# Kernel tuning notes

Hardware: AMD Instinct MI355X
Metric: run time of the kernel (lower is better)

Reference implementation:

```python
import jax, jax.numpy as jnp
import numpy as np

M_DIM, Z_DIM, C = 256, 128, 32
N, L = 512, 384


def setup_inputs() -> dict:
    key = jax.random.key(0)
    ks = jax.random.split(key, 9)
    s = 1.0 / np.sqrt(M_DIM)
    return {
        "m": jax.random.normal(ks[0], (N, L, M_DIM), dtype=jnp.float32),
        "ln_gamma": jnp.ones((M_DIM,), jnp.float32),
        "ln_beta": jnp.zeros((M_DIM,), jnp.float32),
        "w1": jax.random.normal(ks[1], (M_DIM, C), jnp.float32) * s,
        "b1": jnp.zeros((C,), jnp.float32),
        "w2": jax.random.normal(ks[2], (M_DIM, C), jnp.float32) * s,
        "b2": jnp.zeros((C,), jnp.float32),
        "w3": jax.random.normal(ks[3], (C * C, Z_DIM), jnp.float32) * (1.0 / np.sqrt(C * C)),
        "b3": jnp.zeros((Z_DIM,), jnp.float32),
    }


def _layernorm(x, gamma, beta, eps=1e-5):
    mu = jnp.mean(x, axis=-1, keepdims=True)
    var = jnp.mean(jnp.square(x - mu), axis=-1, keepdims=True)
    return (x - mu) * jax.lax.rsqrt(var + eps) * gamma + beta


def reference(m, ln_gamma, ln_beta, w1, b1, w2, b2, w3, b3):
    n = m.shape[0]
    o = _layernorm(m, ln_gamma, ln_beta)          # (N, L, D)
    a = o @ w2 + b2                                # (N, L, C)  linear2
    b = o @ w1 + b1                                # (N, L, C)  linear1
    # mean over N of outer products: reassociated as a single contraction over n
    op = jnp.einsum('nia,njb->ijab', a, b) / n     # (L, L, C, C)
    ll = op.shape[0]
    z = op.reshape(ll, ll, -1) @ w3 + b3           # (L, L, Z)
    return z
```

## Files before the change

kernel.cpp:

```cpp
#include <hip/hip_runtime.h>
#include <hip/hip_bf16.h>
#include <stdint.h>

#define L_DIM 384
#define MD    256
#define CC    32
#define ZD    128
#define NB    512
#define K2    1024
#define MROWS 12288

typedef __attribute__((ext_vector_type(4))) float  f32x4;
typedef __attribute__((ext_vector_type(8))) short  bf16x8;

typedef __attribute__((address_space(1))) unsigned char* gcp;
typedef __attribute__((address_space(3))) unsigned char* lcp;

#define SBAR()  __builtin_amdgcn_s_barrier()
#define LGKM0() asm volatile("s_waitcnt lgkmcnt(0)" ::: "memory")
#define VMW(n)  asm volatile("s_waitcnt vmcnt(" #n ")" ::: "memory")
#define PRIO1() __builtin_amdgcn_s_setprio(1)
#define PRIO0() __builtin_amdgcn_s_setprio(0)

__device__ __forceinline__ unsigned short f2bf(float x) {
    union { float f; unsigned u; } v; v.f = x;
    unsigned r = v.u + 0x7fffu + ((v.u >> 16) & 1u);
    return (unsigned short)(r >> 16);
}

__device__ __forceinline__ uint2 pack4(unsigned short a, unsigned short b,
                                       unsigned short c, unsigned short d) {
    uint2 r; r.x = (unsigned)a | ((unsigned)b << 16);
    r.y = (unsigned)c | ((unsigned)d << 16); return r;
}

__global__ __launch_bounds__(256) void prep_kernel(
    const float* __restrict__ w1, const float* __restrict__ w2,
    const float* __restrict__ w3,
    unsigned short* __restrict__ w3frag, unsigned short* __restrict__ wfrag)
{
    int idx = blockIdx.x * 256 + threadIdx.x;
    if (idx < 131072) {
        int e = idx & 7, lane = (idx >> 3) & 63, zg = (idx >> 9) & 7, ks = idx >> 12;
        int k2p = ks * 32 + ((lane >> 4) << 3) + e;
        int wrow = (k2p & 31) * 32 + (k2p >> 5);
        int z  = zg * 16 + (lane & 15);
        w3frag[idx] = f2bf(w3[(size_t)wrow * ZD + z]);
    } else {
        int j = idx - 131072;
        int e = j & 7, lane = (j >> 3) & 63, nf = (j >> 9) & 3, ks = j >> 11;
        int c = nf * 16 + (lane & 15);
        int d = ks * 32 + ((lane >> 4) << 3) + e;
        float v = (c < CC) ? w2[d * CC + c] : w1[d * CC + (c - CC)];
        wfrag[j] = f2bf(v);
    }
}

__global__ __launch_bounds__(256, 4) void ln_proj_kernel(
    const float* __restrict__ mm, const float* __restrict__ gamma, const float* __restrict__ beta,
    const unsigned short* __restrict__ wfrag,
    const float* __restrict__ b1, const float* __restrict__ b2,
    unsigned short* __restrict__ At, unsigned short* __restrict__ Bt)
{
    __shared__ alignas(16) char o_b[32768];

    const int tid = threadIdx.x, wv = tid >> 6, lane = tid & 63;
    const int l0 = blockIdx.y * 2;
    const int n0 = blockIdx.x * 32;

    const int l_loc = wv >> 1;
    const int nbase = (wv & 1) << 4;
    const int l_g = l0 + l_loc;
    f32x4 g4 = *(const f32x4*)(gamma + lane * 4);
    f32x4 e4 = *(const f32x4*)(beta + lane * 4);

    #pragma unroll 4
    for (int r = 0; r < 16; ++r) {
        int row_loc = wv * 16 + r;
        int n_g = n0 + nbase + r;
        const float* src = mm + ((size_t)n_g * L_DIM + l_g) * MD + lane * 4;
        f32x4 x = *(const f32x4*)src;
        float s  = x[0] + x[1] + x[2] + x[3];
        float s2 = x[0]*x[0] + x[1]*x[1] + x[2]*x[2] + x[3]*x[3];
        #pragma unroll
        for (int off = 32; off > 0; off >>= 1) {
            s  += __shfl_xor(s,  off);
            s2 += __shfl_xor(s2, off);
        }
        float mu  = s * (1.0f / MD);
        float var = s2 * (1.0f / MD) - mu * mu;
        float rs  = rsqrtf(var + 1e-5f);
        unsigned short o0 = f2bf((x[0] - mu) * rs * g4[0] + e4[0]);
        unsigned short o1 = f2bf((x[1] - mu) * rs * g4[1] + e4[1]);
        unsigned short o2 = f2bf((x[2] - mu) * rs * g4[2] + e4[2]);
        unsigned short o3 = f2bf((x[3] - mu) * rs * g4[3] + e4[3]);
        *(uint2*)(o_b + row_loc * 512 + ((lane * 8) ^ ((row_loc & 7) << 4))) = pack4(o0, o1, o2, o3);
    }

    f32x4 acc[4] = {{0,0,0,0},{0,0,0,0},{0,0,0,0},{0,0,0,0}};
    const int lrow = lane & 15;
    const int kq16 = (lane >> 4) << 4;
    const int arow = wv * 16 + lrow;
    #pragma unroll
    for (int ks = 0; ks < 8; ++ks) {
        bf16x8 a = *(const bf16x8*)(o_b + arow * 512 + ((ks * 64 + kq16) ^ ((arow & 7) << 4)));
        #pragma unroll
        for (int nf = 0; nf < 4; ++nf) {
            bf16x8 b = *(const bf16x8*)(wfrag + (size_t)((ks * 4 + nf) * 64 + lane) * 8);
            acc[nf] = __builtin_amdgcn_mfma_f32_16x16x32_bf16(a, b, acc[nf], 0, 0, 0);
        }
    }

    const int rr0 = wv * 16 + ((lane >> 4) << 2);
    const int n_gw = n0 + (rr0 & 31);
    const int l_gw = l0 + (rr0 >> 5);
    #pragma unroll
    for (int nf = 0; nf < 4; ++nf) {
        int c = nf * 16 + lrow;
        float bias = (c < CC) ? b2[c] : b1[c - CC];
        unsigned short ob0 = f2bf(acc[nf][0] + bias);
        unsigned short ob1 = f2bf(acc[nf][1] + bias);
        unsigned short ob2 = f2bf(acc[nf][2] + bias);
        unsigned short ob3 = f2bf(acc[nf][3] + bias);
        unsigned short* dst = ((c < CC) ? At : Bt) + (size_t)(l_gw * CC + (c & 31)) * NB + n_gw;
        *(uint2*)dst = pack4(ob0, ob1, ob2, ob3);
    }
}

__global__ __launch_bounds__(512, 2) void opm_kernel(
    const unsigned short* __restrict__ At, const unsigned short* __restrict__ Bt,
    const unsigned short* __restrict__ w3frag, const float* __restrict__ b3,
    float* __restrict__ Z)
{
    __shared__ alignas(128) char smem[131072];
    char* const Ab = smem;
    char* const Bb = smem + 65536;

    const int tid = threadIdx.x, wv = tid >> 6, lane = tid & 63;

    const int lin = blockIdx.y * 48 + blockIdx.x;
    const int xcd = lin & 7, chunk = lin >> 3;
    const int i0 = (xcd * 6 + (chunk % 6)) * 256;
    const int j0 = (chunk / 6) * 256;

    const int lrow = lane & 15;
    const int kq16 = (lane >> 4) << 4;
    const int wr = (wv >> 2) * 128, wc = (wv & 3) * 64;

    auto stage = [&](const unsigned short* __restrict__ src, int tile0, int kt,
                     int half, int isA) {
        #pragma unroll
        for (int q = 0; q < 2; ++q) {
            int rl0 = q * 64 + wv * 8;
            int rl  = rl0 + (lane >> 3);
            int rc  = isA ? ((rl  & 63) + ((rl  >> 6) << 7) + half * 64)
                          : ((rl  & 31) + ((rl  >> 5) << 6) + half * 32);
            int rc0 = isA ? ((rl0 & 63) + ((rl0 >> 6) << 7) + half * 64)
                          : ((rl0 & 31) + ((rl0 >> 5) << 6) + half * 32);
            const unsigned short* g = src + (size_t)(tile0 + rc) * NB + kt * 64
                                      + (((lane & 7) ^ (lane >> 3)) << 3);
            char* l = (isA ? Ab : Bb) + (kt & 1) * 32768 + rc0 * 128;
            __builtin_amdgcn_global_load_lds((gcp)g, (lcp)l, 16, 0, 0);
        }
    };

    f32x4 acc[8][4] = {};
    bf16x8 av[8], bl[4], bh[4];

    auto rdA = [&](const char* ab, int qrow) {
        #pragma unroll
        for (int mfl = 0; mfl < 4; ++mfl) {
            int row = wr + qrow * 64 + mfl * 16 + lrow;
            const char* p = ab + row * 128;
            av[mfl*2+0] = *(const bf16x8*)(p + ((     kq16) ^ ((row & 7) << 4)));
            av[mfl*2+1] = *(const bf16x8*)(p + ((64 + kq16) ^ ((row & 7) << 4)));
        }
    };
    auto rdB = [&](const char* bb, int qcol, bf16x8* bv) {
        #pragma unroll
        for (int nfl = 0; nfl < 2; ++nfl) {
            int col = wc + qcol * 32 + nfl * 16 + lrow;
            const char* p = bb + col * 128;
            bv[nfl*2+0] = *(const bf16x8*)(p + ((     kq16) ^ ((col & 7) << 4)));
            bv[nfl*2+1] = *(const bf16x8*)(p + ((64 + kq16) ^ ((col & 7) << 4)));
        }
    };
    auto MM = [&](bf16x8* bv, int mbase, int nbase) {
        #pragma unroll
        for (int mfl = 0; mfl < 4; ++mfl)
            #pragma unroll
            for (int nfl = 0; nfl < 2; ++nfl)
                #pragma unroll
                for (int ks = 0; ks < 2; ++ks)
                    acc[mbase+mfl][nbase+nfl] = __builtin_amdgcn_mfma_f32_16x16x32_bf16(
                        av[mfl*2+ks], bv[nfl*2+ks], acc[mbase+mfl][nbase+nfl], 0, 0, 0);
    };

    stage(At, i0, 0, 0, 1); stage(At, i0, 0, 1, 1);
    stage(Bt, j0, 0, 0, 0); stage(Bt, j0, 0, 1, 0);
    stage(At, i0, 1, 0, 1); stage(At, i0, 1, 1, 1);
    stage(Bt, j0, 1, 0, 0); stage(Bt, j0, 1, 1, 0);
    VMW(8);
    SBAR();

    const char* a0 = Ab;           const char* b0 = Bb;
    const char* a1 = Ab + 32768;   const char* b1 = Bb + 32768;

    for (int t = 0; t < 3; ++t) {
        const int ktc = 2*t + 2, ktd = 2*t + 3;
        rdA(a0, 0); rdB(b0, 0, bl);
        SBAR(); LGKM0(); PRIO1(); MM(bl, 0, 0); PRIO0(); SBAR();
        rdB(b0, 1, bh); stage(At, i0, ktc, 0, 1);
        SBAR(); LGKM0(); PRIO1(); MM(bh, 0, 2); PRIO0(); SBAR();
        rdA(a0, 1); stage(Bt, j0, ktc, 0, 0);
        SBAR(); LGKM0(); PRIO1(); MM(bh, 4, 2); PRIO0(); SBAR();
        stage(Bt, j0, ktc, 1, 0);
        SBAR(); LGKM0(); PRIO1(); MM(bl, 4, 0); PRIO0(); VMW(6); SBAR();
        rdA(a1, 0); rdB(b1, 0, bl); stage(At, i0, ktc, 1, 1);
        SBAR(); LGKM0(); PRIO1(); MM(bl, 0, 0); PRIO0(); SBAR();
        rdB(b1, 1, bh); stage(At, i0, ktd, 0, 1);
        SBAR(); LGKM0(); PRIO1(); MM(bh, 0, 2); PRIO0(); SBAR();
        rdA(a1, 1); stage(Bt, j0, ktd, 0, 0);
        SBAR(); LGKM0(); PRIO1(); MM(bh, 4, 2); PRIO0(); SBAR();
        stage(Bt, j0, ktd, 1, 0); stage(At, i0, ktd, 1, 1);
        SBAR(); LGKM0(); PRIO1(); MM(bl, 4, 0); PRIO0(); VMW(8); SBAR();
    }

    rdA(a0, 0); rdB(b0, 0, bl);
    SBAR(); LGKM0(); PRIO1(); MM(bl, 0, 0); PRIO0(); SBAR();
    rdB(b0, 1, bh);
    SBAR(); LGKM0(); PRIO1(); MM(bh, 0, 2); PRIO0(); SBAR();
    rdA(a0, 1);
    SBAR(); LGKM0(); PRIO1(); MM(bh, 4, 2); PRIO0(); SBAR();
    SBAR(); LGKM0(); PRIO1(); MM(bl, 4, 0); PRIO0(); VMW(0); SBAR();
    rdA(a1, 0); rdB(b1, 0, bl);
    SBAR(); LGKM0(); PRIO1(); MM(bl, 0, 0); PRIO0(); SBAR();
    rdB(b1, 1, bh);
    SBAR(); LGKM0(); PRIO1(); MM(bh, 0, 2); PRIO0(); SBAR();
    rdA(a1, 1);
    SBAR(); LGKM0(); PRIO1(); MM(bh, 4, 2); PRIO0(); SBAR();
    SBAR(); LGKM0(); PRIO1(); MM(bl, 4, 0); PRIO0(); SBAR();

    char* const opb = smem;
    const int lq = lane >> 4;
    const int zg = wv;
    const int zc = zg * 16 + lrow;

    auto ldW = [&](int ks) -> bf16x8 {
        return *(const bf16x8*)(w3frag + (size_t)((ks * 8 + zg) * 64 + lane) * 8);
    };
    auto ldP = [&](int rg, int ks) -> bf16x8 {
        int row = rg * 16 + lrow;
        int g = ks * 4 + lq;
        int b = g >> 2, jj = g & 3;
        int inner = (b * 64 + jj * 16) ^ (((b >> 1) & 7) << 4) ^ ((row & 7) << 4);
        return *(const bf16x8*)(opb + row * 2048 + inner);
    };

    bf16x8 wR0 = ldW(0), wR1 = ldW(1), wR2 = ldW(2), wR3 = ldW(3);

    const float scale = 1.0f / (float)NB;
    #pragma unroll
    for (int mf = 0; mf < 8; ++mf) {
        #pragma unroll
        for (int nf = 0; nf < 4; ++nf) {
            int col = wc + nf * 16 + lrow;
            int bcol = col & 31;
            int row = wr + mf * 16 + ((lane >> 4) << 2);
            int pl = ((row >> 5) << 3) | (col >> 5);
            int a0e = row & 31;
            int inner = (bcol * 64 + a0e * 2) ^ (((bcol >> 1) & 7) << 4) ^ ((pl & 7) << 4);
            *(uint2*)(opb + pl * 2048 + inner) =
                pack4(f2bf(acc[mf][nf][0] * scale), f2bf(acc[mf][nf][1] * scale),
                      f2bf(acc[mf][nf][2] * scale), f2bf(acc[mf][nf][3] * scale));
        }
    }
    __syncthreads();

    f32x4 accP[4] = {};
    bf16x8 pA[4], pB[4];
    #pragma unroll
    for (int r = 0; r < 4; ++r) pA[r] = ldP(r, 0);
    #pragma unroll
    for (int r = 0; r < 4; ++r) pB[r] = ldP(r, 1);

    #pragma unroll
    for (int ks = 0; ks < 32; ++ks) {
        bf16x8 w = ((ks & 3) == 0) ? wR0 : ((ks & 3) == 1) ? wR1
                 : ((ks & 3) == 2) ? wR2 : wR3;
        bf16x8* pc = (ks & 1) ? pB : pA;
        PRIO1();
        accP[0] = __builtin_amdgcn_mfma_f32_16x16x32_bf16(pc[0], w, accP[0], 0, 0, 0);
        accP[1] = __builtin_amdgcn_mfma_f32_16x16x32_bf16(pc[1], w, accP[1], 0, 0, 0);
        accP[2] = __builtin_amdgcn_mfma_f32_16x16x32_bf16(pc[2], w, accP[2], 0, 0, 0);
        accP[3] = __builtin_amdgcn_mfma_f32_16x16x32_bf16(pc[3], w, accP[3], 0, 0, 0);
        PRIO0();
        if (ks + 4 < 32) {
            if ((ks & 3) == 0)      wR0 = ldW(ks + 4);
            else if ((ks & 3) == 1) wR1 = ldW(ks + 4);
            else if ((ks & 3) == 2) wR2 = ldW(ks + 4);
            else                    wR3 = ldW(ks + 4);
        }
        if (ks + 2 < 32) {
            #pragma unroll
            for (int r = 0; r < 4; ++r) pc[r] = ldP(r, ks + 2);
        }
    }

    const int pq = (lane >> 4) << 2;
    const float bias = b3[zc];
    #pragma unroll
    for (int pf = 0; pf < 4; ++pf) {
        #pragma unroll
        for (int rr = 0; rr < 4; ++rr) {
            int pl = pf * 16 + pq + rr;
            int ii = (i0 >> 5) + (pl >> 3);
            int jj = (j0 >> 5) + (pl & 7);
            Z[((size_t)ii * L_DIM + jj) * ZD + zc] = accP[pf][rr] + bias;
        }
    }
}

extern "C" void kernel_launch(void* const* d_in, const int* in_sizes, int n_in,
                              void* d_out, int out_size, void* d_ws, size_t ws_size,
                              hipStream_t stream)
{
    const float* mm    = (const float*)d_in[0];
    const float* gamma = (const float*)d_in[1];
    const float* beta  = (const float*)d_in[2];
    const float* w1    = (const float*)d_in[3];
    const float* b1    = (const float*)d_in[4];
    const float* w2    = (const float*)d_in[5];
    const float* b2    = (const float*)d_in[6];
    const float* w3    = (const float*)d_in[7];
    const float* b3    = (const float*)d_in[8];

    unsigned short* At     = (unsigned short*)d_ws;
    unsigned short* Bt     = At + (size_t)MROWS * NB;
    unsigned short* w3frag = Bt + (size_t)MROWS * NB;
    unsigned short* wfrag  = w3frag + 131072;

    prep_kernel<<<576, 256, 0, stream>>>(w1, w2, w3, w3frag, wfrag);
    ln_proj_kernel<<<dim3(16, 192), 256, 0, stream>>>(mm, gamma, beta, wfrag, b1, b2, At, Bt);
    opm_kernel<<<dim3(48, 48), 512, 0, stream>>>(At, Bt, w3frag, b3, (float*)d_out);
}
```

Before: 260.0 us.

## Make OPM kernel persistent with cross-tile prefetch and split epilogue

Converts the outer-product GEMM kernel from a 48x48 grid of one-tile blocks into a persistent kernel of 256 blocks, each looping over 9 output tiles. During the last k-step of each tile it prefetches the first k-slice of the next tile, so global loads overlap the epilogue instead of stalling at each block start. The w3 projection epilogue is split into two halves that reuse a smaller shared-memory region, so the staging buffers for the next tile are not overwritten. This adds more barriers and a more complex schedule, and it fixes the tile count at 9 per block.

```diff
diff --git a/kernel.cpp b/kernel.cpp
--- a/kernel.cpp
+++ b/kernel.cpp
@@ -137,14 +137,9 @@
     char* const Bb = smem + 65536;
 
     const int tid = threadIdx.x, wv = tid >> 6, lane = tid & 63;
-
-    const int lin = blockIdx.y * 48 + blockIdx.x;
-    const int xcd = lin & 7, chunk = lin >> 3;
-    const int i0 = (xcd * 6 + (chunk % 6)) * 256;
-    const int j0 = (chunk / 6) * 256;
-
     const int lrow = lane & 15;
     const int kq16 = (lane >> 4) << 4;
+    const int lq   = lane >> 4;
     const int wr = (wv >> 2) * 128, wc = (wv & 3) * 64;
 
     auto stage = [&](const unsigned short* __restrict__ src, int tile0, int kt,
@@ -164,7 +159,7 @@
         }
     };
 
-    f32x4 acc[8][4] = {};
+    f32x4 acc[8][4];
     bf16x8 av[8], bl[4], bh[4];
 
     auto rdA = [&](const char* ab, int qrow) {
@@ -196,127 +191,136 @@
                         av[mfl*2+ks], bv[nfl*2+ks], acc[mbase+mfl][nbase+nfl], 0, 0, 0);
     };
 
-    stage(At, i0, 0, 0, 1); stage(At, i0, 0, 1, 1);
-    stage(Bt, j0, 0, 0, 0); stage(Bt, j0, 0, 1, 0);
-    stage(At, i0, 1, 0, 1); stage(At, i0, 1, 1, 1);
-    stage(Bt, j0, 1, 0, 0); stage(Bt, j0, 1, 1, 0);
-    VMW(8);
-    SBAR();
-
-    const char* a0 = Ab;           const char* b0 = Bb;
-    const char* a1 = Ab + 32768;   const char* b1 = Bb + 32768;
-
-    for (int t = 0; t < 3; ++t) {
-        const int ktc = 2*t + 2, ktd = 2*t + 3;
-        rdA(a0, 0); rdB(b0, 0, bl);
-        SBAR(); LGKM0(); PRIO1(); MM(bl, 0, 0); PRIO0(); SBAR();
-        rdB(b0, 1, bh); stage(At, i0, ktc, 0, 1);
-        SBAR(); LGKM0(); PRIO1(); MM(bh, 0, 2); PRIO0(); SBAR();
-        rdA(a0, 1); stage(Bt, j0, ktc, 0, 0);
-        SBAR(); LGKM0(); PRIO1(); MM(bh, 4, 2); PRIO0(); SBAR();
-        stage(Bt, j0, ktc, 1, 0);
-        SBAR(); LGKM0(); PRIO1(); MM(bl, 4, 0); PRIO0(); VMW(6); SBAR();
-        rdA(a1, 0); rdB(b1, 0, bl); stage(At, i0, ktc, 1, 1);
-        SBAR(); LGKM0(); PRIO1(); MM(bl, 0, 0); PRIO0(); SBAR();
-        rdB(b1, 1, bh); stage(At, i0, ktd, 0, 1);
-        SBAR(); LGKM0(); PRIO1(); MM(bh, 0, 2); PRIO0(); SBAR();
-        rdA(a1, 1); stage(Bt, j0, ktd, 0, 0);
-        SBAR(); LGKM0(); PRIO1(); MM(bh, 4, 2); PRIO0(); SBAR();
-        stage(Bt, j0, ktd, 1, 0); stage(At, i0, ktd, 1, 1);
-        SBAR(); LGKM0(); PRIO1(); MM(bl, 4, 0); PRIO0(); VMW(8); SBAR();
-    }
-
-    rdA(a0, 0); rdB(b0, 0, bl);
-    SBAR(); LGKM0(); PRIO1(); MM(bl, 0, 0); PRIO0(); SBAR();
-    rdB(b0, 1, bh);
-    SBAR(); LGKM0(); PRIO1(); MM(bh, 0, 2); PRIO0(); SBAR();
-    rdA(a0, 1);
-    SBAR(); LGKM0(); PRIO1(); MM(bh, 4, 2); PRIO0(); SBAR();
-    SBAR(); LGKM0(); PRIO1(); MM(bl, 4, 0); PRIO0(); VMW(0); SBAR();
-    rdA(a1, 0); rdB(b1, 0, bl);
-    SBAR(); LGKM0(); PRIO1(); MM(bl, 0, 0); PRIO0(); SBAR();
-    rdB(b1, 1, bh);
-    SBAR(); LGKM0(); PRIO1(); MM(bh, 0, 2); PRIO0(); SBAR();
-    rdA(a1, 1);
-    SBAR(); LGKM0(); PRIO1(); MM(bh, 4, 2); PRIO0(); SBAR();
-    SBAR(); LGKM0(); PRIO1(); MM(bl, 4, 0); PRIO0(); SBAR();
-
-    char* const opb = smem;
-    const int lq = lane >> 4;
-    const int zg = wv;
-    const int zc = zg * 16 + lrow;
-
-    auto ldW = [&](int ks) -> bf16x8 {
-        return *(const bf16x8*)(w3frag + (size_t)((ks * 8 + zg) * 64 + lane) * 8);
-    };
-    auto ldP = [&](int rg, int ks) -> bf16x8 {
-        int row = rg * 16 + lrow;
-        int g = ks * 4 + lq;
-        int b = g >> 2, jj = g & 3;
-        int inner = (b * 64 + jj * 16) ^ (((b >> 1) & 7) << 4) ^ ((row & 7) << 4);
-        return *(const bf16x8*)(opb + row * 2048 + inner);
-    };
-
-    bf16x8 wR0 = ldW(0), wR1 = ldW(1), wR2 = ldW(2), wR3 = ldW(3);
-
-    const float scale = 1.0f / (float)NB;
-    #pragma unroll
-    for (int mf = 0; mf < 8; ++mf) {
-        #pragma unroll
-        for (int nf = 0; nf < 4; ++nf) {
-            int col = wc + nf * 16 + lrow;
-            int bcol = col & 31;
-            int row = wr + mf * 16 + ((lane >> 4) << 2);
-            int pl = ((row >> 5) << 3) | (col >> 5);
-            int a0e = row & 31;
-            int inner = (bcol * 64 + a0e * 2) ^ (((bcol >> 1) & 7) << 4) ^ ((pl & 7) << 4);
-            *(uint2*)(opb + pl * 2048 + inner) =
-                pack4(f2bf(acc[mf][nf][0] * scale), f2bf(acc[mf][nf][1] * scale),
-                      f2bf(acc[mf][nf][2] * scale), f2bf(acc[mf][nf][3] * scale));
-        }
-    }
-    __syncthreads();
-
-    f32x4 accP[4] = {};
-    bf16x8 pA[4], pB[4];
-    #pragma unroll
-    for (int r = 0; r < 4; ++r) pA[r] = ldP(r, 0);
-    #pragma unroll
-    for (int r = 0; r < 4; ++r) pB[r] = ldP(r, 1);
-
-    #pragma unroll
-    for (int ks = 0; ks < 32; ++ks) {
-        bf16x8 w = ((ks & 3) == 0) ? wR0 : ((ks & 3) == 1) ? wR1
-                 : ((ks & 3) == 2) ? wR2 : wR3;
-        bf16x8* pc = (ks & 1) ? pB : pA;
-        PRIO1();
-        accP[0] = __builtin_amdgcn_mfma_f32_16x16x32_bf16(pc[0], w, accP[0], 0, 0, 0);
-        accP[1] = __builtin_amdgcn_mfma_f32_16x16x32_bf16(pc[1], w, accP[1], 0, 0, 0);
-        accP[2] = __builtin_amdgcn_mfma_f32_16x16x32_bf16(pc[2], w, accP[2], 0, 0, 0);
-        accP[3] = __builtin_amdgcn_mfma_f32_16x16x32_bf16(pc[3], w, accP[3], 0, 0, 0);
-        PRIO0();
-        if (ks + 4 < 32) {
-            if ((ks & 3) == 0)      wR0 = ldW(ks + 4);
-            else if ((ks & 3) == 1) wR1 = ldW(ks + 4);
-            else if ((ks & 3) == 2) wR2 = ldW(ks + 4);
-            else                    wR3 = ldW(ks + 4);
-        }
-        if (ks + 2 < 32) {
-            #pragma unroll
-            for (int r = 0; r < 4; ++r) pc[r] = ldP(r, ks + 2);
-        }
-    }
-
-    const int pq = (lane >> 4) << 2;
-    const float bias = b3[zc];
-    #pragma unroll
-    for (int pf = 0; pf < 4; ++pf) {
-        #pragma unroll
-        for (int rr = 0; rr < 4; ++rr) {
-            int pl = pf * 16 + pq + rr;
-            int ii = (i0 >> 5) + (pl >> 3);
-            int jj = (j0 >> 5) + (pl & 7);
-            Z[((size_t)ii * L_DIM + jj) * ZD + zc] = accP[pf][rr] + bias;
+    for (int it = 0; it < 9; ++it) {
+        const int lin = it * 256 + blockIdx.x;
+        const int xcd = lin & 7, chunk = lin >> 3;
+        const int i0 = (xcd * 6 + (chunk % 6)) * 256;
+        const int j0 = (chunk / 6) * 256;
+        const int chn = chunk + 32;
+        const int ni0 = (xcd * 6 + (chn % 6)) * 256;
+        const int nj0 = ((chn / 6) % 48) * 256;
+        const bool hn = (it < 8);
+
+        #pragma unroll
+        for (int mf = 0; mf < 8; ++mf)
+            #pragma unroll
+            for (int nf = 0; nf < 4; ++nf)
+                acc[mf][nf] = (f32x4){0.f, 0.f, 0.f, 0.f};
+
+        if (it == 0) {
+            stage(At, i0, 0, 0, 1); stage(Bt, j0, 0, 0, 0);
+            stage(At, i0, 0, 1, 1); stage(Bt, j0, 0, 1, 0);
+            VMW(0); SBAR();
+        } else {
+            VMW(8); SBAR();
+        }
+
+        #pragma unroll
+        for (int k = 0; k < 8; ++k) {
+            const char* ab = Ab + (k & 1) * 32768;
+            const char* bb = Bb + (k & 1) * 32768;
+            rdA(ab, 0); rdB(bb, 0, bl);
+            if (k == 0)              { stage(At, i0, 1, 0, 1); stage(Bt, j0, 1, 0, 0); }
+            else if (k <= 5)         { stage(At, i0, k + 2, 0, 1); }
+            else if (k == 7 && hn)   { stage(At, ni0, 0, 0, 1); }
+            SBAR(); LGKM0(); PRIO1(); MM(bl, 0, 0); PRIO0(); SBAR();
+            rdB(bb, 1, bh);
+            if (k == 0)              { stage(At, i0, 1, 1, 1); stage(Bt, j0, 1, 1, 0); }
+            else if (k <= 5)         { stage(Bt, j0, k + 2, 0, 0); }
+            else if (k == 7 && hn)   { stage(Bt, nj0, 0, 0, 0); }
+            SBAR(); LGKM0(); PRIO1(); MM(bh, 0, 2); PRIO0(); SBAR();
+            rdA(ab, 1);
+            if (k == 0)              { stage(At, i0, 2, 0, 1); stage(Bt, j0, 2, 0, 0); }
+            else if (k <= 5)         { stage(At, i0, k + 2, 1, 1); }
+            else if (k == 7 && hn)   { stage(At, ni0, 0, 1, 1); }
+            SBAR(); LGKM0(); PRIO1(); MM(bh, 4, 2); PRIO0(); SBAR();
+            if (k == 0)              { stage(At, i0, 2, 1, 1); stage(Bt, j0, 2, 1, 0); }
+            else if (k <= 5)         { stage(Bt, j0, k + 2, 1, 0); }
+            else if (k == 7 && hn)   { stage(Bt, nj0, 0, 1, 0); }
+            SBAR(); LGKM0(); PRIO1(); MM(bl, 4, 0); PRIO0();
+            if (k <= 5) { VMW(8); }
+            else if (k == 6) { VMW(0); }
+            SBAR();
+        }
+
+        const float scale = 1.0f / (float)NB;
+        const int zg = wv;
+        const int zc = zg * 16 + lrow;
+        const float bias = b3[zc];
+        const int pq = (lane >> 4) << 2;
+
+        auto ldW = [&](int ks) -> bf16x8 {
+            return *(const bf16x8*)(w3frag + (size_t)((ks * 8 + zg) * 64 + lane) * 8);
+        };
+        auto ldP = [&](int rg, int ks) -> bf16x8 {
+            int g = ks * 4 + lq;
+            int b = g >> 2, jj = g & 3;
+            int inner = (b * 64 + jj * 16) ^ (((b >> 1) & 7) << 4) ^ ((lrow & 7) << 4);
+            return *(const bf16x8*)(smem + 32768 + rg * 65536 + lrow * 2048 + inner);
+        };
+
+        #pragma unroll
+        for (int h = 0; h < 2; ++h) {
+            bf16x8 wR0 = ldW(0), wR1 = ldW(1), wR2 = ldW(2), wR3 = ldW(3);
+
+            if ((wv >> 2) == h) {
+                #pragma unroll
+                for (int mf = 0; mf < 8; ++mf) {
+                    #pragma unroll
+                    for (int nf = 0; nf < 4; ++nf) {
+                        int col  = wc + nf * 16 + lrow;
+                        int bcol = col & 31;
+                        int rowl = mf * 16 + pq;
+                        int pl   = ((rowl >> 5) << 3) | (col >> 5);
+                        int inner = (bcol * 64 + (rowl & 31) * 2)
+                                    ^ (((bcol >> 1) & 7) << 4) ^ ((pl & 7) << 4);
+                        *(uint2*)(smem + 32768 + (pl >> 4) * 65536 + (pl & 15) * 2048 + inner) =
+                            pack4(f2bf(acc[mf][nf][0] * scale), f2bf(acc[mf][nf][1] * scale),
+                                  f2bf(acc[mf][nf][2] * scale), f2bf(acc[mf][nf][3] * scale));
+                    }
+                }
+            }
+            LGKM0(); SBAR();
+
+            f32x4 accP[2] = {};
+            bf16x8 pA[2], pB[2];
+            #pragma unroll
+            for (int r = 0; r < 2; ++r) pA[r] = ldP(r, 0);
+            #pragma unroll
+            for (int r = 0; r < 2; ++r) pB[r] = ldP(r, 1);
+
+            #pragma unroll
+            for (int ks = 0; ks < 32; ++ks) {
+                bf16x8 w = ((ks & 3) == 0) ? wR0 : ((ks & 3) == 1) ? wR1
+                         : ((ks & 3) == 2) ? wR2 : wR3;
+                bf16x8* pc = (ks & 1) ? pB : pA;
+                PRIO1();
+                accP[0] = __builtin_amdgcn_mfma_f32_16x16x32_bf16(pc[0], w, accP[0], 0, 0, 0);
+                accP[1] = __builtin_amdgcn_mfma_f32_16x16x32_bf16(pc[1], w, accP[1], 0, 0, 0);
+                PRIO0();
+                if (ks + 4 < 32) {
+                    if ((ks & 3) == 0)      wR0 = ldW(ks + 4);
+                    else if ((ks & 3) == 1) wR1 = ldW(ks + 4);
+                    else if ((ks & 3) == 2) wR2 = ldW(ks + 4);
+                    else                    wR3 = ldW(ks + 4);
+                }
+                if (ks + 2 < 32) {
+                    #pragma unroll
+                    for (int r = 0; r < 2; ++r) pc[r] = ldP(r, ks + 2);
+                }
+            }
+
+            #pragma unroll
+            for (int pf = 0; pf < 2; ++pf) {
+                #pragma unroll
+                for (int rr = 0; rr < 4; ++rr) {
+                    int pl = h * 32 + pf * 16 + pq + rr;
+                    int ii = (i0 >> 5) + (pl >> 3);
+                    int jj = (j0 >> 5) + (pl & 7);
+                    Z[((size_t)ii * L_DIM + jj) * ZD + zc] = accP[pf][rr] + bias;
+                }
+            }
+            if (h == 0) { LGKM0(); SBAR(); }
         }
     }
 }
@@ -342,5 +346,5 @@
 
     prep_kernel<<<576, 256, 0, stream>>>(w1, w2, w3, w3frag, wfrag);
     ln_proj_kernel<<<dim3(16, 192), 256, 0, stream>>>(mm, gamma, beta, wfrag, b1, b2, At, Bt);
-    opm_kernel<<<dim3(48, 48), 512, 0, stream>>>(At, Bt, w3frag, b3, (float*)d_out);
-}
+    opm_kernel<<<256, 512, 0, stream>>>(At, Bt, w3frag, b3, (float*)d_out);
+}
```

Result: slower. 543.3 us (+108.9%).
